# Performance work log

Measured on AMD Instinct MI355X. Metric: run time of the kernel, lower is better.

## Reference

```python
import jax, jax.numpy as jnp
import numpy as np

D_MODEL = 1024
NHEAD = 16
DH = D_MODEL // NHEAD  # 64
B, S = 4, 2048
SCALE = float(np.sqrt(D_MODEL))  # note: sqrt(d_model), not sqrt(dh)


def setup_inputs() -> dict:
    key = jax.random.key(0)
    ks = jax.random.split(key, 8)
    inputs = jax.random.normal(ks[0], (B, S, D_MODEL), dtype=jnp.float32)
    mask = jax.random.normal(ks[1], (B, S, S), dtype=jnp.float32) * 0.1
    # Linear weights stored as [in, out] so y = x @ W + b (equivalent to torch x @ W.T + b)
    std = 1.0 / np.sqrt(D_MODEL)
    Wq = jax.random.normal(ks[2], (D_MODEL, DH), dtype=jnp.float32) * std
    Wk = jax.random.normal(ks[3], (D_MODEL, DH), dtype=jnp.float32) * std
    Wv = jax.random.normal(ks[4], (D_MODEL, DH), dtype=jnp.float32) * std
    bq = jnp.zeros((DH,), dtype=jnp.float32)
    bk = jnp.zeros((DH,), dtype=jnp.float32)
    bv = jnp.zeros((DH,), dtype=jnp.float32)
    return {"inputs": inputs, "mask": mask, "Wq": Wq, "bq": bq,
            "Wk": Wk, "bk": bk, "Wv": Wv, "bv": bv}


def reference(inputs, mask, Wq, bq, Wk, bk, Wv, bv):
    # Projections: [B,S,d_model] -> [B,S,dh]
    Q = inputs @ Wq + bq
    K = inputs @ Wk + bk
    V = inputs @ Wv + bv
    # scores: [B, S_q, S_k]
    scores = jnp.einsum("bqd,bkd->bqk", Q, K) / SCALE
    # Faithful quirk: softmax over dim=1 (the QUERY axis), not the key axis
    probs = jax.nn.softmax(scores, axis=1)
    # Faithful quirk: mask added AFTER softmax
    A = jnp.einsum("bqk,bkd->bqd", probs + mask, V)
    return A
```

## Files before the change

kernel.cpp:

```cpp
#include <hip/hip_runtime.h>

#define NB 4
#define SS 2048
#define DMODEL 1024
#define DHEAD 64

typedef __bf16 bf16x8 __attribute__((ext_vector_type(8)));
typedef __bf16 bf16x4 __attribute__((ext_vector_type(4)));
typedef float f32x4 __attribute__((ext_vector_type(4)));

#define MFMA16(a, b, c) __builtin_amdgcn_mfma_f32_16x16x32_bf16((a), (b), (c), 0, 0, 0)

__global__ __launch_bounds__(256) void k0_wt3(
    const float* __restrict__ Wq, const float* __restrict__ Wk,
    const float* __restrict__ Wv, __bf16* __restrict__ Wt3)
{
    int idx = blockIdx.x * 256 + threadIdx.x;
    int kc = idx / 768;
    int rem = idx - kc * 768;
    int f = rem >> 6;
    int lane = rem & 63;
    int g = lane >> 4, l15 = lane & 15;
    int mode = f >> 2, nt = f & 3;
    const float* W = (mode == 0) ? Wq : (mode == 1 ? Wk : Wv);
    const float s = (mode == 0) ? 0.03125f : 1.0f;
    int n = nt * 16 + l15;
    int k = kc * 32 + g * 8;
    bf16x8 o;
    #pragma unroll
    for (int i = 0; i < 8; ++i)
        o[i] = (__bf16)(W[(size_t)(k + i) * DHEAD + n] * s);
    *(bf16x8*)(Wt3 + (size_t)idx * 8) = o;
}

#define XST 1032
__global__ __launch_bounds__(256) void k1_fused(
    const float* __restrict__ x, const __bf16* __restrict__ Wt3,
    const float* __restrict__ bq, const float* __restrict__ bk,
    const float* __restrict__ bv,
    __bf16* __restrict__ Qo, __bf16* __restrict__ Ko, __bf16* __restrict__ Vt)
{
    __shared__ char smem[36864];
    __bf16* stage = (__bf16*)smem;
    const int tid = threadIdx.x;
    const int wid = tid >> 6;
    const int lane = tid & 63;
    const int l15 = lane & 15;
    const int g = lane >> 4;
    const int row0 = blockIdx.x * 16;

    {
        const float* xsrc = x + (size_t)row0 * DMODEL;
        #pragma unroll
        for (int it = 0; it < 16; ++it) {
            int idx = it * 256 + tid;
            int row = idx >> 8;
            int col = (idx & 255) * 4;
            f32x4 v = *(const f32x4*)(xsrc + (size_t)row * DMODEL + col);
            bf16x4 b4;
            #pragma unroll
            for (int i = 0; i < 4; ++i) b4[i] = (__bf16)v[i];
            *(bf16x4*)(stage + row * XST + col) = b4;
        }
    }
    __syncthreads();

    f32x4 acc[12];
    #pragma unroll
    for (int f = 0; f < 12; ++f) acc[f] = (f32x4){0.f, 0.f, 0.f, 0.f};

    #pragma unroll
    for (int c = 0; c < 8; ++c) {
        bf16x8 af = *(const bf16x8*)(stage + l15 * XST + wid * 256 + c * 32 + g * 8);
        const int kc = wid * 8 + c;
        #pragma unroll
        for (int f = 0; f < 12; ++f) {
            bf16x8 bfr = *(const bf16x8*)(Wt3 + (((size_t)kc * 12 + f) << 9) + lane * 8);
            acc[f] = MFMA16(af, bfr, acc[f]);
        }
    }
    __syncthreads();
    f32x4* red = (f32x4*)smem;
    if (wid != 0) {
        #pragma unroll
        for (int f = 0; f < 12; ++f) red[((wid - 1) * 12 + f) * 64 + lane] = acc[f];
    }
    __syncthreads();
    if (wid == 0) {
        const int b  = row0 >> 11;
        const int s0 = row0 & 2047;
        #pragma unroll
        for (int f = 0; f < 12; ++f) {
            f32x4 a = acc[f] + red[(0 * 12 + f) * 64 + lane]
                    + red[(1 * 12 + f) * 64 + lane] + red[(2 * 12 + f) * 64 + lane];
            const int md = f >> 2, nt = f & 3;
            const int n = nt * 16 + l15;
            const float* bias = (md == 0) ? bq : (md == 1 ? bk : bv);
            const float bscale = (md == 0) ? 0.03125f : 1.0f;
            float bvl = bias[n] * bscale;
            #pragma unroll
            for (int r = 0; r < 4; ++r) {
                float o = a[r] + bvl;
                int sr = s0 + g * 4 + r;
                if (md == 0)      Qo[((size_t)b * SS + sr) * DHEAD + n] = (__bf16)o;
                else if (md == 1) Ko[((size_t)b * SS + sr) * DHEAD + n] = (__bf16)o;
                else              Vt[((size_t)b * DHEAD + n) * SS + sr] = (__bf16)o;
            }
        }
    }
}

#define QST 72
__global__ __launch_bounds__(256) void k2_cs(
    const __bf16* __restrict__ Qb, const __bf16* __restrict__ Kb,
    float* __restrict__ partial)
{
    __shared__ __bf16 qt[128 * QST];
    const int tid = threadIdx.x;
    const int wid = tid >> 6;
    const int lane = tid & 63;
    const int l15 = lane & 15;
    const int g = lane >> 4;
    const int bx = blockIdx.x;
    const int b  = bx >> 8;
    const int rem = bx & 255;
    const int kg = rem >> 4;
    const int qs = rem & 15;
    const int k0 = kg * 128 + wid * 32;

    {
        const __bf16* qsrc = Qb + ((size_t)(b * SS + qs * 128)) * DHEAD;
        #pragma unroll
        for (int it = 0; it < 4; ++it) {
            int idx = it * 256 + tid;
            int row = idx >> 3;
            int col = (idx & 7) * 8;
            *(bf16x8*)(qt + row * QST + col) = *(const bf16x8*)(qsrc + (size_t)idx * 8);
        }
    }

    const __bf16* kp0 = Kb + ((size_t)(b * SS + k0 + l15)) * DHEAD + g * 8;
    bf16x8 ka00 = *(const bf16x8*)(kp0);
    bf16x8 ka01 = *(const bf16x8*)(kp0 + 32);
    const __bf16* kp1 = kp0 + 16 * DHEAD;
    bf16x8 ka10 = *(const bf16x8*)(kp1);
    bf16x8 ka11 = *(const bf16x8*)(kp1 + 32);
    __syncthreads();

    f32x4 cs0 = (f32x4){0.f, 0.f, 0.f, 0.f};
    f32x4 cs1 = (f32x4){0.f, 0.f, 0.f, 0.f};

    #pragma unroll 2
    for (int j = 0; j < 8; ++j) {
        const __bf16* qr = qt + (j * 16 + l15) * QST + g * 8;
        bf16x8 qb0 = *(const bf16x8*)(qr);
        bf16x8 qb1 = *(const bf16x8*)(qr + 32);
        f32x4 s0 = (f32x4){0.f, 0.f, 0.f, 0.f};
        s0 = MFMA16(ka00, qb0, s0);
        s0 = MFMA16(ka01, qb1, s0);
        f32x4 s1 = (f32x4){0.f, 0.f, 0.f, 0.f};
        s1 = MFMA16(ka10, qb0, s1);
        s1 = MFMA16(ka11, qb1, s1);
        #pragma unroll
        for (int r = 0; r < 4; ++r) {
            cs0[r] += __expf(s0[r]);
            cs1[r] += __expf(s1[r]);
        }
    }
    #pragma unroll
    for (int off = 1; off < 16; off <<= 1) {
        #pragma unroll
        for (int r = 0; r < 4; ++r) {
            cs0[r] += __shfl_xor(cs0[r], off);
            cs1[r] += __shfl_xor(cs1[r], off);
        }
    }
    if (l15 == 0) {
        float* pp = partial + (size_t)qs * (NB * SS) + b * SS + k0 + 4 * g;
        *(f32x4*)(pp)      = cs0;
        *(f32x4*)(pp + 16) = cs1;
    }
}

#define KST 72
#define VST 136
#define MTS 136
__global__ __launch_bounds__(256) void kab(
    const __bf16* __restrict__ Qb, const __bf16* __restrict__ Kb,
    const __bf16* __restrict__ Vt, const float* __restrict__ mask,
    const float* __restrict__ part, float* __restrict__ out)
{
    __shared__ char smem[48384];
    __bf16* kt = (__bf16*)smem;
    __bf16* vt = (__bf16*)(smem + 18432);
    __bf16* mt = (__bf16*)(smem + 18432 + 17408);
    float*  rl = (float*)(smem + 18432 + 17408 + 4352);
    const int tid = threadIdx.x;
    const int wid = tid >> 6;
    const int lane = tid & 63;
    const int l15 = lane & 15;
    const int g = lane >> 4;
    const int b  = blockIdx.x >> 7;
    const int q0 = (blockIdx.x & 127) * 16;

    {
        const int k = tid * 8;
        f32x4 sa = (f32x4){0.f, 0.f, 0.f, 0.f};
        f32x4 sb = (f32x4){0.f, 0.f, 0.f, 0.f};
        #pragma unroll
        for (int qs = 0; qs < 16; ++qs) {
            const float* pp = part + (size_t)qs * (NB * SS) + b * SS + k;
            sa += *(const f32x4*)(pp);
            sb += *(const f32x4*)(pp + 4);
        }
        f32x4 ra, rb;
        #pragma unroll
        for (int r = 0; r < 4; ++r) { ra[r] = 1.0f / sa[r]; rb[r] = 1.0f / sb[r]; }
        *(f32x4*)(rl + k) = ra;
        *(f32x4*)(rl + k + 4) = rb;
    }

    const __bf16* qp = Qb + ((size_t)(b * SS + q0 + l15)) * DHEAD + g * 8;
    bf16x8 qb0 = *(const bf16x8*)(qp);
    bf16x8 qb1 = *(const bf16x8*)(qp + 32);

    f32x4 acc[4];
    #pragma unroll
    for (int nt = 0; nt < 4; ++nt) acc[nt] = (f32x4){0.f, 0.f, 0.f, 0.f};

    for (int cc = 0; cc < 16; ++cc) {
        __syncthreads();
        {
            const __bf16* ksrc = Kb + ((size_t)b * SS + cc * 128) * DHEAD;
            #pragma unroll
            for (int it = 0; it < 4; ++it) {
                int idx = it * 256 + tid;
                int row = idx >> 3;
                int col = (idx & 7) * 8;
                *(bf16x8*)(kt + row * KST + col) = *(const bf16x8*)(ksrc + (size_t)idx * 8);
            }
            const __bf16* vsrc = Vt + (size_t)b * DHEAD * SS + cc * 128;
            #pragma unroll
            for (int it = 0; it < 4; ++it) {
                int idx = it * 256 + tid;
                int row = idx >> 4;
                int col = (idx & 15) * 8;
                *(bf16x8*)(vt + row * VST + col) = *(const bf16x8*)(vsrc + (size_t)row * SS + col);
            }
            const float* msrc = mask + ((size_t)(b * SS + q0)) * SS + cc * 128;
            #pragma unroll
            for (int it = 0; it < 2; ++it) {
                int idx = it * 256 + tid;
                int row = idx >> 5;
                int col = (idx & 31) * 4;
                f32x4 v = *(const f32x4*)(msrc + (size_t)row * SS + col);
                bf16x4 b4;
                #pragma unroll
                for (int i = 0; i < 4; ++i) b4[i] = (__bf16)v[i];
                *(bf16x4*)(mt + row * MTS + col) = b4;
            }
        }
        __syncthreads();

        const int kl = wid * 32;
        const __bf16* kr0 = kt + (kl + l15) * KST + g * 8;
        bf16x8 ka00 = *(const bf16x8*)(kr0);
        bf16x8 ka01 = *(const bf16x8*)(kr0 + 32);
        const __bf16* kr1 = kr0 + 16 * KST;
        bf16x8 ka10 = *(const bf16x8*)(kr1);
        bf16x8 ka11 = *(const bf16x8*)(kr1 + 32);

        f32x4 s0 = (f32x4){0.f, 0.f, 0.f, 0.f};
        s0 = MFMA16(ka00, qb0, s0);
        s0 = MFMA16(ka01, qb1, s0);
        f32x4 s1 = (f32x4){0.f, 0.f, 0.f, 0.f};
        s1 = MFMA16(ka10, qb0, s1);
        s1 = MFMA16(ka11, qb1, s1);

        const int kbase = cc * 128 + kl;
        f32x4 rv0 = *(const f32x4*)(rl + kbase + 4 * g);
        f32x4 rv1 = *(const f32x4*)(rl + kbase + 16 + 4 * g);
        f32x4 e0, e1;
        #pragma unroll
        for (int r = 0; r < 4; ++r) {
            e0[r] = __expf(s0[r]) * rv0[r];
            e1[r] = __expf(s1[r]) * rv1[r];
        }
        bf16x8 mv = *(const bf16x8*)(mt + l15 * MTS + kl + g * 8);
        bf16x8 af;
        #pragma unroll
        for (int i = 0; i < 8; ++i) {
            int src = l15 + 16 * ((2 * g + (i >> 2)) & 3);
            float v0 = __shfl(e0[i & 3], src);
            float v1 = __shfl(e1[i & 3], src);
            af[i] = (__bf16)((g < 2 ? v0 : v1) + (float)mv[i]);
        }
        #pragma unroll
        for (int nt = 0; nt < 4; ++nt) {
            bf16x8 vb = *(const bf16x8*)(vt + (nt * 16 + l15) * VST + kl + g * 8);
            acc[nt] = MFMA16(af, vb, acc[nt]);
        }
    }
    __syncthreads();
    f32x4* red = (f32x4*)smem;
    #pragma unroll
    for (int nt = 0; nt < 4; ++nt) red[(wid * 4 + nt) * 64 + lane] = acc[nt];
    __syncthreads();
    if (wid == 0) {
        #pragma unroll
        for (int nt = 0; nt < 4; ++nt) {
            f32x4 a = red[(0 * 4 + nt) * 64 + lane] + red[(1 * 4 + nt) * 64 + lane]
                    + red[(2 * 4 + nt) * 64 + lane] + red[(3 * 4 + nt) * 64 + lane];
            #pragma unroll
            for (int r = 0; r < 4; ++r)
                out[((size_t)(b * SS + q0 + g * 4 + r)) * DHEAD + nt * 16 + l15] = a[r];
        }
    }
}

extern "C" void kernel_launch(void* const* d_in, const int* in_sizes, int n_in,
                              void* d_out, int out_size, void* d_ws, size_t ws_size,
                              hipStream_t stream)
{
    const float* x    = (const float*)d_in[0];
    const float* mask = (const float*)d_in[1];
    const float* Wq   = (const float*)d_in[2];
    const float* bq   = (const float*)d_in[3];
    const float* Wk   = (const float*)d_in[4];
    const float* bk   = (const float*)d_in[5];
    const float* Wv   = (const float*)d_in[6];
    const float* bv   = (const float*)d_in[7];
    float* out = (float*)d_out;

    char* ws = (char*)d_ws;
    __bf16* Qbf  = (__bf16*)(ws);
    __bf16* Kbf  = (__bf16*)(ws + (1u << 20));
    __bf16* Vt   = (__bf16*)(ws + (2u << 20));
    float*  part = (float*)(ws + (3u << 20));
    __bf16* Wt3  = (__bf16*)(ws + (3u << 20) + (512u << 10));

    k0_wt3<<<96, 256, 0, stream>>>(Wq, Wk, Wv, Wt3);
    k1_fused<<<512, 256, 0, stream>>>(x, Wt3, bq, bk, bv, Qbf, Kbf, Vt);
    k2_cs<<<1024, 256, 0, stream>>>(Qbf, Kbf, part);
    kab<<<512, 256, 0, stream>>>(Qbf, Kbf, Vt, mask, part, out);
}
```

Baseline: 65.72 us.

## Store K and V in MFMA fragment layout and read fragments directly from global

The projection kernel now writes K and V in a pre-swizzled MFMA fragment layout, so each lane loads its operand fragment with a single contiguous 16-byte read. The attention kernel drops its per-chunk LDS staging of K, V and mask along with the two barriers per chunk. It instead loads the whole 16x2048 mask tile into LDS once up front, and each wave walks its own 512-key slice, reading K and V fragments straight from global memory. This removes repeated LDS round trips and synchronisation, at the cost of about 74KB of LDS per block (lower occupancy) and scattered 2-byte stores in the projection epilogue.

```diff
diff --git a/kernel.cpp b/kernel.cpp
--- a/kernel.cpp
+++ b/kernel.cpp
@@ -10,6 +10,7 @@
 typedef float f32x4 __attribute__((ext_vector_type(4)));
 
 #define MFMA16(a, b, c) __builtin_amdgcn_mfma_f32_16x16x32_bf16((a), (b), (c), 0, 0, 0)
+
 
 __global__ __launch_bounds__(256) void k0_wt3(
     const float* __restrict__ Wq, const float* __restrict__ Wk,
@@ -38,7 +39,7 @@
     const float* __restrict__ x, const __bf16* __restrict__ Wt3,
     const float* __restrict__ bq, const float* __restrict__ bk,
     const float* __restrict__ bv,
-    __bf16* __restrict__ Qo, __bf16* __restrict__ Ko, __bf16* __restrict__ Vt)
+    __bf16* __restrict__ Qo, __bf16* __restrict__ Kb3, __bf16* __restrict__ Vt3)
 {
     __shared__ char smem[36864];
     __bf16* stage = (__bf16*)smem;
@@ -89,6 +90,7 @@
     if (wid == 0) {
         const int b  = row0 >> 11;
         const int s0 = row0 & 2047;
+        const int soff = (s0 >> 3) & 2;
         #pragma unroll
         for (int f = 0; f < 12; ++f) {
             f32x4 a = acc[f] + red[(0 * 12 + f) * 64 + lane]
@@ -102,9 +104,17 @@
             for (int r = 0; r < 4; ++r) {
                 float o = a[r] + bvl;
                 int sr = s0 + g * 4 + r;
-                if (md == 0)      Qo[((size_t)b * SS + sr) * DHEAD + n] = (__bf16)o;
-                else if (md == 1) Ko[((size_t)b * SS + sr) * DHEAD + n] = (__bf16)o;
-                else              Vt[((size_t)b * DHEAD + n) * SS + sr] = (__bf16)o;
+                if (md == 0) {
+                    Qo[((size_t)b * SS + sr) * DHEAD + n] = (__bf16)o;
+                } else if (md == 1) {
+                    size_t fid = (size_t)b * 256 + (s0 >> 4) * 2 + (nt >> 1);
+                    int ln = ((nt & 1) * 2 + (l15 >> 3)) * 16 + g * 4 + r;
+                    Kb3[(fid << 9) + ln * 8 + (l15 & 7)] = (__bf16)o;
+                } else {
+                    size_t fid = (size_t)b * 256 + (s0 >> 5) * 4 + nt;
+                    int ln = (soff + ((g * 4 + r) >> 3)) * 16 + l15;
+                    Vt3[(fid << 9) + ln * 8 + ((g * 4 + r) & 7)] = (__bf16)o;
+                }
             }
         }
     }
@@ -112,7 +122,7 @@
 
 #define QST 72
 __global__ __launch_bounds__(256) void k2_cs(
-    const __bf16* __restrict__ Qb, const __bf16* __restrict__ Kb,
+    const __bf16* __restrict__ Qb, const __bf16* __restrict__ Kb3,
     float* __restrict__ partial)
 {
     __shared__ __bf16 qt[128 * QST];
@@ -139,12 +149,11 @@
         }
     }
 
-    const __bf16* kp0 = Kb + ((size_t)(b * SS + k0 + l15)) * DHEAD + g * 8;
-    bf16x8 ka00 = *(const bf16x8*)(kp0);
-    bf16x8 ka01 = *(const bf16x8*)(kp0 + 32);
-    const __bf16* kp1 = kp0 + 16 * DHEAD;
-    bf16x8 ka10 = *(const bf16x8*)(kp1);
-    bf16x8 ka11 = *(const bf16x8*)(kp1 + 32);
+    const __bf16* kfr = Kb3 + (((size_t)b * 256 + (k0 >> 4) * 2) << 9) + lane * 8;
+    bf16x8 ka00 = *(const bf16x8*)(kfr);
+    bf16x8 ka01 = *(const bf16x8*)(kfr + 512);
+    bf16x8 ka10 = *(const bf16x8*)(kfr + 1024);
+    bf16x8 ka11 = *(const bf16x8*)(kfr + 1536);
     __syncthreads();
 
     f32x4 cs0 = (f32x4){0.f, 0.f, 0.f, 0.f};
@@ -182,19 +191,15 @@
     }
 }
 
-#define KST 72
-#define VST 136
-#define MTS 136
+#define MST 2056
 __global__ __launch_bounds__(256) void kab(
-    const __bf16* __restrict__ Qb, const __bf16* __restrict__ Kb,
-    const __bf16* __restrict__ Vt, const float* __restrict__ mask,
+    const __bf16* __restrict__ Qb, const __bf16* __restrict__ Kb3,
+    const __bf16* __restrict__ Vt3, const float* __restrict__ mask,
     const float* __restrict__ part, float* __restrict__ out)
 {
-    __shared__ char smem[48384];
-    __bf16* kt = (__bf16*)smem;
-    __bf16* vt = (__bf16*)(smem + 18432);
-    __bf16* mt = (__bf16*)(smem + 18432 + 17408);
-    float*  rl = (float*)(smem + 18432 + 17408 + 4352);
+    __shared__ char smem[16 * MST * 2 + 8192];
+    __bf16* mt = (__bf16*)smem;
+    float*  rl = (float*)(smem + 16 * MST * 2);
     const int tid = threadIdx.x;
     const int wid = tid >> 6;
     const int lane = tid & 63;
@@ -219,56 +224,43 @@
         *(f32x4*)(rl + k) = ra;
         *(f32x4*)(rl + k + 4) = rb;
     }
+    {
+        const float* msrc = mask + ((size_t)(b * SS + q0)) * SS;
+        #pragma unroll
+        for (int it = 0; it < 32; ++it) {
+            int idx = it * 256 + tid;
+            int row = idx >> 9;
+            int col = (idx & 511) * 4;
+            f32x4 v = *(const f32x4*)(msrc + (size_t)row * SS + col);
+            bf16x4 b4;
+            #pragma unroll
+            for (int i = 0; i < 4; ++i) b4[i] = (__bf16)v[i];
+            *(bf16x4*)(mt + row * MST + col) = b4;
+        }
+    }
 
     const __bf16* qp = Qb + ((size_t)(b * SS + q0 + l15)) * DHEAD + g * 8;
     bf16x8 qb0 = *(const bf16x8*)(qp);
     bf16x8 qb1 = *(const bf16x8*)(qp + 32);
+    __syncthreads();
 
     f32x4 acc[4];
     #pragma unroll
     for (int nt = 0; nt < 4; ++nt) acc[nt] = (f32x4){0.f, 0.f, 0.f, 0.f};
 
-    for (int cc = 0; cc < 16; ++cc) {
-        __syncthreads();
-        {
-            const __bf16* ksrc = Kb + ((size_t)b * SS + cc * 128) * DHEAD;
-            #pragma unroll
-            for (int it = 0; it < 4; ++it) {
-                int idx = it * 256 + tid;
-                int row = idx >> 3;
-                int col = (idx & 7) * 8;
-                *(bf16x8*)(kt + row * KST + col) = *(const bf16x8*)(ksrc + (size_t)idx * 8);
-            }
-            const __bf16* vsrc = Vt + (size_t)b * DHEAD * SS + cc * 128;
-            #pragma unroll
-            for (int it = 0; it < 4; ++it) {
-                int idx = it * 256 + tid;
-                int row = idx >> 4;
-                int col = (idx & 15) * 8;
-                *(bf16x8*)(vt + row * VST + col) = *(const bf16x8*)(vsrc + (size_t)row * SS + col);
-            }
-            const float* msrc = mask + ((size_t)(b * SS + q0)) * SS + cc * 128;
-            #pragma unroll
-            for (int it = 0; it < 2; ++it) {
-                int idx = it * 256 + tid;
-                int row = idx >> 5;
-                int col = (idx & 31) * 4;
-                f32x4 v = *(const f32x4*)(msrc + (size_t)row * SS + col);
-                bf16x4 b4;
-                #pragma unroll
-                for (int i = 0; i < 4; ++i) b4[i] = (__bf16)v[i];
-                *(bf16x4*)(mt + row * MTS + col) = b4;
-            }
-        }
-        __syncthreads();
-
-        const int kl = wid * 32;
-        const __bf16* kr0 = kt + (kl + l15) * KST + g * 8;
-        bf16x8 ka00 = *(const bf16x8*)(kr0);
-        bf16x8 ka01 = *(const bf16x8*)(kr0 + 32);
-        const __bf16* kr1 = kr0 + 16 * KST;
-        bf16x8 ka10 = *(const bf16x8*)(kr1);
-        bf16x8 ka11 = *(const bf16x8*)(kr1 + 32);
+    #pragma unroll 2
+    for (int st = 0; st < 16; ++st) {
+        const int kbase = wid * 512 + st * 32;
+        const __bf16* kfr = Kb3 + (((size_t)b * 256 + (kbase >> 4) * 2) << 9) + lane * 8;
+        bf16x8 ka00 = *(const bf16x8*)(kfr);
+        bf16x8 ka01 = *(const bf16x8*)(kfr + 512);
+        bf16x8 ka10 = *(const bf16x8*)(kfr + 1024);
+        bf16x8 ka11 = *(const bf16x8*)(kfr + 1536);
+        const __bf16* vfr = Vt3 + (((size_t)b * 256 + (kbase >> 5) * 4) << 9) + lane * 8;
+        bf16x8 vb0 = *(const bf16x8*)(vfr);
+        bf16x8 vb1 = *(const bf16x8*)(vfr + 512);
+        bf16x8 vb2 = *(const bf16x8*)(vfr + 1024);
+        bf16x8 vb3 = *(const bf16x8*)(vfr + 1536);
 
         f32x4 s0 = (f32x4){0.f, 0.f, 0.f, 0.f};
         s0 = MFMA16(ka00, qb0, s0);
@@ -277,7 +269,6 @@
         s1 = MFMA16(ka10, qb0, s1);
         s1 = MFMA16(ka11, qb1, s1);
 
-        const int kbase = cc * 128 + kl;
         f32x4 rv0 = *(const f32x4*)(rl + kbase + 4 * g);
         f32x4 rv1 = *(const f32x4*)(rl + kbase + 16 + 4 * g);
         f32x4 e0, e1;
@@ -286,7 +277,7 @@
             e0[r] = __expf(s0[r]) * rv0[r];
             e1[r] = __expf(s1[r]) * rv1[r];
         }
-        bf16x8 mv = *(const bf16x8*)(mt + l15 * MTS + kl + g * 8);
+        bf16x8 mv = *(const bf16x8*)(mt + l15 * MST + kbase + g * 8);
         bf16x8 af;
         #pragma unroll
         for (int i = 0; i < 8; ++i) {
@@ -295,11 +286,10 @@
             float v1 = __shfl(e1[i & 3], src);
             af[i] = (__bf16)((g < 2 ? v0 : v1) + (float)mv[i]);
         }
-        #pragma unroll
-        for (int nt = 0; nt < 4; ++nt) {
-            bf16x8 vb = *(const bf16x8*)(vt + (nt * 16 + l15) * VST + kl + g * 8);
-            acc[nt] = MFMA16(af, vb, acc[nt]);
-        }
+        acc[0] = MFMA16(af, vb0, acc[0]);
+        acc[1] = MFMA16(af, vb1, acc[1]);
+        acc[2] = MFMA16(af, vb2, acc[2]);
+        acc[3] = MFMA16(af, vb3, acc[3]);
     }
     __syncthreads();
     f32x4* red = (f32x4*)smem;
@@ -334,13 +324,13 @@
 
     char* ws = (char*)d_ws;
     __bf16* Qbf  = (__bf16*)(ws);
-    __bf16* Kbf  = (__bf16*)(ws + (1u << 20));
-    __bf16* Vt   = (__bf16*)(ws + (2u << 20));
+    __bf16* Kb3  = (__bf16*)(ws + (1u << 20));
+    __bf16* Vt3  = (__bf16*)(ws + (2u << 20));
     float*  part = (float*)(ws + (3u << 20));
     __bf16* Wt3  = (__bf16*)(ws + (3u << 20) + (512u << 10));
 
     k0_wt3<<<96, 256, 0, stream>>>(Wq, Wk, Wv, Wt3);
-    k1_fused<<<512, 256, 0, stream>>>(x, Wt3, bq, bk, bv, Qbf, Kbf, Vt);
-    k2_cs<<<1024, 256, 0, stream>>>(Qbf, Kbf, part);
-    kab<<<512, 256, 0, stream>>>(Qbf, Kbf, Vt, mask, part, out);
-}
+    k1_fused<<<512, 256, 0, stream>>>(x, Wt3, bq, bk, bv, Qbf, Kb3, Vt3);
+    k2_cs<<<1024, 256, 0, stream>>>(Qbf, Kb3, part);
+    kab<<<512, 256, 0, stream>>>(Qbf, Kb3, Vt3, mask, part, out);
+}
```

New measurement: 57.37 us. 12.7% less time.
